# Optimization experiments

Hardware: AMD Instinct MI355X
Metric: run time of the kernel (lower is better)

Reference implementation:

```python
import jax, jax.numpy as jnp
import numpy as np

W, H = 1920, 1080
WEIGHT = 0.2          # self.weight
CONT_W = 0.1          # continuity_weight
RANK_M = 1e-4         # ranking_margin
CONT_M = 1e-4         # continuity_margin
SAMPLE_RATIO = 0.25
R = 3                 # knn_crop_radius
PAD_VAL = -1000000.0


def setup_inputs() -> dict:
    key = jax.random.key(0)
    k1, k2, k3 = jax.random.split(key, 3)
    return {
        "target_depths": jax.random.uniform(k1, (1, H * W), dtype=jnp.float32) * 100.0,
        "render_depths": jax.random.uniform(k2, (H * W,), dtype=jnp.float32) * 100.0,
        "valid_mask": jax.random.randint(k3, (1, H * W, 1), 0, 2, dtype=jnp.int32),
        "width": W,
        "height": H,
    }


def _sample_depth_loss_indices(depths, width, height, valid_mask, n_samples,
                               rank_patch_size, r, key):
    win = 2 * r + 1                      # 7
    top_n = int(0.3 * win * win + 1)     # 15
    ks = jax.random.split(key, 5)
    sy = jax.random.randint(ks[0], (n_samples, 1), 0, height - rank_patch_size)
    sx = jax.random.randint(ks[1], (n_samples, 1), 0, width - rank_patch_size)
    sy = sy + jax.random.randint(ks[2], (n_samples, 2), 0, rank_patch_size)
    sx = sx + jax.random.randint(ks[3], (n_samples, 2), 0, rank_patch_size)
    sample_idx = sy * width + sx                               # (n, 2)
    sampled_depth = depths[0][sample_idx]                      # (n, 2)

    padded = jnp.pad(depths.reshape(height, width), r, constant_values=PAD_VAL)
    dy = jnp.repeat(jnp.arange(win), win)                      # (49,) row offsets
    dx = jnp.tile(jnp.arange(win), win)                        # (49,) col offsets
    # padded coords: (y - r + dy) + r == y + dy
    py = sy[..., None] + dy                                    # (n, 2, 49)
    px = sx[..., None] + dx
    depth_crops = padded[py, px]                               # (n, 2, 49)

    sorted_crop_idx = jnp.argsort(jnp.abs(depth_crops - sampled_depth[..., None]), axis=-1)
    nbr_sample = jax.random.randint(ks[4], (n_samples, 2, 1), 1, top_n)
    rel = jnp.take_along_axis(sorted_crop_idx, nbr_sample, axis=-1)[..., 0]  # (n, 2)
    ny = sy - r + rel // win
    nx = sx - r + rel % win
    neighbours_idx = ny * width + nx                           # (n, 2)

    vm = valid_mask[0].astype(bool)                            # (H*W, C)
    samples_mask = vm[sample_idx].any(-1).all(-1)              # (n,)
    neighbours_mask = vm[neighbours_idx].any(-1).all(-1)
    full_mask = samples_mask & neighbours_mask

    # per-pair descending sort by sampled target depth
    order = jnp.argsort(-sampled_depth, axis=-1)
    s_sorted = jnp.take_along_axis(sample_idx, order, axis=-1)
    n_sorted = jnp.take_along_axis(neighbours_idx, order, axis=-1)
    idx4 = jnp.concatenate([s_sorted, n_sorted], axis=-1)      # (n, 4)
    return idx4, full_mask


def reference(target_depths, render_depths, valid_mask, width, height):
    n_samples = int(width * height * SAMPLE_RATIO)
    rank_patch_size = width // 8
    idx4, mask = _sample_depth_loss_indices(
        target_depths, width, height, valid_mask, n_samples, rank_patch_size,
        R, jax.random.key(42))
    d = render_depths[idx4].reshape(-1, 2, 2)                  # (n, 2, 2)
    rank = jnp.maximum(d[:, 0, 0] - d[:, 0, 1] + RANK_M, 0.0)  # (n,)
    cont = jnp.maximum(jnp.abs(d[:, 0, :] - d[:, 1, :]) - CONT_M, 0.0)  # (n, 2)
    # masked means == torch's boolean filtering followed by .mean()
    m = mask.astype(rank.dtype)
    denom = jnp.maximum(m.sum(), 1.0)
    rank_mean = (rank * m).sum() / denom
    cont_mean = (cont * m[:, None]).sum() / (denom * 2.0)
    return jnp.stack([WEIGHT * rank_mean, WEIGHT * CONT_W * cont_mean])
```

## Files before the change

### kernel.cpp

```cpp
#include <hip/hip_runtime.h>
#include <stdint.h>


#define IMG_W 1920
#define IMG_H 1080
#define N_SAMP 518400
#define PAD_VAL (-1000000.0f)

struct Keys { uint32_t k[5][2][2]; };

static __host__ __device__ inline void tf2x32(uint32_t k0, uint32_t k1,
                                              uint32_t x0, uint32_t x1,
                                              uint32_t& o0, uint32_t& o1)
{
  const uint32_t ks2 = k0 ^ k1 ^ 0x1BD11BDAu;
  x0 += k0; x1 += k1;
#define TFR(r) { x0 += x1; x1 = (x1 << (r)) | (x1 >> (32 - (r))); x1 ^= x0; }
  TFR(13) TFR(15) TFR(26) TFR(6)
  x0 += k1;  x1 += ks2 + 1u;
  TFR(17) TFR(29) TFR(16) TFR(24)
  x0 += ks2; x1 += k0 + 2u;
  TFR(13) TFR(15) TFR(26) TFR(6)
  x0 += k0;  x1 += k1 + 3u;
  TFR(17) TFR(29) TFR(16) TFR(24)
  x0 += k1;  x1 += ks2 + 4u;
  TFR(13) TFR(15) TFR(26) TFR(6)
  x0 += ks2; x1 += k0 + 5u;
#undef TFR
  o0 = x0; o1 = x1;
}

__device__ __forceinline__ uint32_t jrbits(const uint32_t kk[2], uint32_t f)
{
  uint32_t a, b;
  tf2x32(kk[0], kk[1], 0u, f, a, b);
  return a ^ b;
}

__device__ __forceinline__ uint32_t jrandint(const Keys& K, int r, uint32_t f,
                                             uint32_t span)
{
  const uint32_t hi = jrbits(K.k[r][0], f);
  const uint32_t lo = jrbits(K.k[r][1], f);
  uint32_t m = 65536u % span;
  m = (m * m) % span;
  return ((hi % span) * m + (lo % span)) % span;
}

static void compute_keys(Keys& K)
{
  uint32_t ks[5][2];
  for (uint32_t t = 0; t < 5; t++) {
    uint32_t a, b; tf2x32(0u, 42u, 0u, t, a, b);
    ks[t][0] = a; ks[t][1] = b;
  }
  for (int r = 0; r < 5; r++) {
    uint32_t a, b;
    tf2x32(ks[r][0], ks[r][1], 0u, 0u, a, b); K.k[r][0][0] = a; K.k[r][0][1] = b;
    tf2x32(ks[r][0], ks[r][1], 0u, 1u, a, b); K.k[r][1][0] = a; K.k[r][1][1] = b;
  }
}

__device__ __forceinline__ int crop_neighbor(const float* __restrict__ tgt,
                                             int sy, int sx, float sd,
                                             uint32_t nbr)
{
  float v[7][8];
  const bool interior = (sy >= 3) && (sy <= IMG_H - 4) &&
                        (sx >= 3) && (sx <= IMG_W - 4);
  if (interior) {
    const float* p = tgt + (sy - 3) * IMG_W + (sx - 3);
#pragma unroll
    for (int r = 0; r < 7; r++)
#pragma unroll
      for (int c = 0; c < 8; c++)
        v[r][c] = p[r * IMG_W + c];
  } else {
#pragma unroll
    for (int r = 0; r < 7; r++) {
      const int yy = sy - 3 + r;
      const bool rok = (yy >= 0) && (yy < IMG_H);
#pragma unroll
      for (int c = 0; c < 8; c++) {
        const int xx = sx - 3 + c;
        const bool ok = rok && (c < 7) && (xx >= 0) && (xx < IMG_W);
        v[r][c] = ok ? tgt[yy * IMG_W + xx] : PAD_VAL;
      }
    }
  }

  uint32_t arr[15];
#pragma unroll
  for (int t = 0; t < 15; t++) arr[t] = 0xFFFFFFFFu;

#pragma unroll
  for (int r = 0; r < 7; r++) {
#pragma unroll
    for (int c = 0; c < 7; c++) {
      const int q = r * 7 + c;
      uint32_t key = (__float_as_uint(v[r][c] - sd) & 0x7FFFFFC0u) | (uint32_t)q;
      const int depth = (q + 1 < 15) ? (q + 1) : 15;
#pragma unroll
      for (int t = 0; t < 15; t++) {
        if (t < depth) {
          const uint32_t lo = min(key, arr[t]);
          const uint32_t hi = max(key, arr[t]);
          arr[t] = lo; key = hi;
        }
      }
    }
  }

  uint32_t relkey = 0;
#pragma unroll
  for (int t = 1; t < 15; t++)
    if ((uint32_t)t == nbr) relkey = arr[t];
  const uint32_t rel = relkey & 63u;
  const int ny = sy - 3 + (int)(rel / 7u);
  const int nx = sx - 3 + (int)(rel % 7u);
  return ny * IMG_W + nx;
}

__global__ __launch_bounds__(256, 2) void gs_fused(
    const float* __restrict__ tgt,
    const float* __restrict__ rnd,
    const int*   __restrict__ vmask,
    float* __restrict__ acc,
    Keys K)
{
  __shared__ unsigned long long ent[256];
  __shared__ float    res_sd[512];
  __shared__ int      res_ni[512];
  __shared__ uint32_t scnt[4];
  __shared__ float    partial[12];

  const uint32_t tid  = threadIdx.x;
  const uint32_t lane = tid & 63u;
  const uint32_t wave = tid >> 6;
  const uint32_t ui   = blockIdx.x * 256u + tid;

  const uint32_t syb = jrandint(K, 0, ui, 840u);
  const uint32_t sxb = jrandint(K, 1, ui, 1680u);
  const uint32_t sy0 = syb + jrandint(K, 2, 2u * ui,      240u);
  const uint32_t sy1 = syb + jrandint(K, 2, 2u * ui + 1u, 240u);
  const uint32_t sx0 = sxb + jrandint(K, 3, 2u * ui,      240u);
  const uint32_t sx1 = sxb + jrandint(K, 3, 2u * ui + 1u, 240u);
  const bool ok = (vmask[sy0 * IMG_W + sx0] != 0) &&
                  (vmask[sy1 * IMG_W + sx1] != 0);

  const unsigned long long ball = __ballot(ok);
  if (lane == 0) scnt[wave] = (uint32_t)__popcll(ball);
  __syncthreads();

  uint32_t base = 0;
#pragma unroll
  for (uint32_t w = 0; w < 4; w++) if (w < wave) base += scnt[w];
  const uint32_t nsurv = scnt[0] + scnt[1] + scnt[2] + scnt[3];

  if (ok) {
    const uint32_t pos = base + (uint32_t)__popcll(ball & ((1ull << lane) - 1ull));
    ent[pos] = ((unsigned long long)ui  << 44) |
               ((unsigned long long)sy0 << 33) | ((unsigned long long)sx0 << 22) |
               ((unsigned long long)sy1 << 11) |  (unsigned long long)sx1;
  }
  __syncthreads();

  for (uint32_t t = tid; t < 2u * nsurv; t += 256u) {
    const unsigned long long e = ent[t >> 1];
    const int jj = (int)(t & 1u);
    const uint32_t eui = (uint32_t)(e >> 44);
    const int sy = jj ? (int)((e >> 11) & 2047u) : (int)((e >> 33) & 2047u);
    const int sx = jj ? (int)( e        & 2047u) : (int)((e >> 22) & 2047u);

    const float sd = tgt[sy * IMG_W + sx];
    const uint32_t nbr = 1u + jrandint(K, 4, 2u * eui + (uint32_t)jj, 14u);
    const int nidx = crop_neighbor(tgt, sy, sx, sd, nbr);
    res_sd[t] = sd;
    res_ni[t] = (vmask[nidx] != 0) ? nidx : -1;
  }
  __syncthreads();

  float rank_c = 0.f, cont_c = 0.f, cnt_c = 0.f;
  for (uint32_t s = tid; s < nsurv; s += 256u) {
    const int n0 = res_ni[2u * s], n1 = res_ni[2u * s + 1u];
    if ((n0 >= 0) && (n1 >= 0)) {
      const unsigned long long e = ent[s];
      const int esy0 = (int)((e >> 33) & 2047u), esx0 = (int)((e >> 22) & 2047u);
      const int esy1 = (int)((e >> 11) & 2047u), esx1 = (int)( e        & 2047u);
      const float r0 = rnd[esy0 * IMG_W + esx0];
      const float r1 = rnd[esy1 * IMG_W + esx1];
      const float q0 = rnd[n0], q1 = rnd[n1];
      const float sd0 = res_sd[2u * s], sd1 = res_sd[2u * s + 1u];
      const bool keep = sd0 >= sd1;
      const float ra = keep ? r0 : r1;
      const float rb = keep ? r1 : r0;
      rank_c += fmaxf(ra - rb + 1e-4f, 0.f);
      cont_c += fmaxf(fabsf(r0 - q0) - 1e-4f, 0.f)
              + fmaxf(fabsf(r1 - q1) - 1e-4f, 0.f);
      cnt_c  += 1.f;
    }
  }

#pragma unroll
  for (int off = 32; off > 0; off >>= 1) {
    rank_c += __shfl_down(rank_c, off);
    cont_c += __shfl_down(cont_c, off);
    cnt_c  += __shfl_down(cnt_c, off);
  }
  if (lane == 0) {
    partial[wave * 3 + 0] = rank_c;
    partial[wave * 3 + 1] = cont_c;
    partial[wave * 3 + 2] = cnt_c;
  }
  __syncthreads();
  if (tid < 3) {
    const float s = partial[tid] + partial[3 + tid] +
                    partial[6 + tid] + partial[9 + tid];
    atomicAdd(acc + tid, s);
  }
}

__global__ void gs_finalize(const float* __restrict__ acc, float* __restrict__ out)
{
  const float denom = fmaxf(acc[2], 1.0f);
  out[0] = 0.2f * (acc[0] / denom);
  out[1] = 0.2f * 0.1f * (acc[1] / (denom * 2.0f));
}

extern "C" void kernel_launch(void* const* d_in, const int* in_sizes, int n_in,
                              void* d_out, int out_size, void* d_ws, size_t ws_size,
                              hipStream_t stream)
{
  (void)in_sizes; (void)n_in; (void)out_size; (void)ws_size;
  const float* tgt   = (const float*)d_in[0];
  const float* rnd   = (const float*)d_in[1];
  const int*   vmask = (const int*)d_in[2];
  float* out = (float*)d_out;
  float* acc = (float*)d_ws;

  Keys K;
  compute_keys(K);

  hipMemsetAsync(acc, 0, 16, stream);
  gs_fused<<<N_SAMP / 256, 256, 0, stream>>>(tgt, rnd, vmask, acc, K);
  gs_finalize<<<1, 1, 0, stream>>>(acc, out);
}
```

Baseline: 62.69 us.

## Bitpack valid mask and process two sample batches per block

```diff
diff --git a/kernel.cpp b/kernel.cpp
--- a/kernel.cpp
+++ b/kernel.cpp
@@ -4,6 +4,7 @@
 
 #define IMG_W 1920
 #define IMG_H 1080
+#define N_PIX (IMG_W * IMG_H)
 #define N_SAMP 518400
 #define PAD_VAL (-1000000.0f)
 
@@ -61,20 +62,34 @@
   }
 }
 
+__device__ __forceinline__ bool validat(const unsigned long long* __restrict__ vb,
+                                        const int* __restrict__ vm, uint32_t idx)
+{
+  if (vb) return ((vb[idx >> 6] >> (idx & 63u)) & 1ull) != 0ull;
+  return vm[idx] != 0;
+}
+
+__global__ __launch_bounds__(256) void gs_bitpack(
+    const int* __restrict__ vmask,
+    unsigned long long* __restrict__ vbits)
+{
+  const uint32_t gid = blockIdx.x * 256u + threadIdx.x;
+  const unsigned long long ball = __ballot(vmask[gid] != 0);
+  if ((threadIdx.x & 63u) == 0) vbits[gid >> 6] = ball;
+}
+
 __device__ __forceinline__ int crop_neighbor(const float* __restrict__ tgt,
                                              int sy, int sx, float sd,
                                              uint32_t nbr)
 {
   float v[7][8];
   const bool interior = (sy >= 3) && (sy <= IMG_H - 4) &&
-                        (sx >= 3) && (sx <= IMG_W - 4);
+                        (sx >= 3) && (sx <= IMG_W - 5);
   if (interior) {
     const float* p = tgt + (sy - 3) * IMG_W + (sx - 3);
 #pragma unroll
     for (int r = 0; r < 7; r++)
-#pragma unroll
-      for (int c = 0; c < 8; c++)
-        v[r][c] = p[r * IMG_W + c];
+      __builtin_memcpy(&v[r][0], p + r * IMG_W, 32);
   } else {
 #pragma unroll
     for (int r = 0; r < 7; r++) {
@@ -83,11 +98,12 @@
 #pragma unroll
       for (int c = 0; c < 8; c++) {
         const int xx = sx - 3 + c;
-        const bool ok = rok && (c < 7) && (xx >= 0) && (xx < IMG_W);
-        v[r][c] = ok ? tgt[yy * IMG_W + xx] : PAD_VAL;
+        const bool okc = rok && (c < 7) && (xx >= 0) && (xx < IMG_W);
+        v[r][c] = okc ? tgt[yy * IMG_W + xx] : PAD_VAL;
       }
     }
   }
+  __builtin_amdgcn_sched_barrier(0);
 
   uint32_t arr[15];
 #pragma unroll
@@ -125,58 +141,76 @@
     const float* __restrict__ tgt,
     const float* __restrict__ rnd,
     const int*   __restrict__ vmask,
+    const unsigned long long* __restrict__ vbits,
     float* __restrict__ acc,
     Keys K)
 {
-  __shared__ unsigned long long ent[256];
-  __shared__ float    res_sd[512];
-  __shared__ int      res_ni[512];
-  __shared__ uint32_t scnt[4];
+  __shared__ unsigned long long ent[512];
+  __shared__ float    res_sd[1024];
+  __shared__ int      res_ni[1024];
+  __shared__ uint32_t scnt[8];
   __shared__ float    partial[12];
 
   const uint32_t tid  = threadIdx.x;
   const uint32_t lane = tid & 63u;
   const uint32_t wave = tid >> 6;
-  const uint32_t ui   = blockIdx.x * 256u + tid;
-
-  const uint32_t syb = jrandint(K, 0, ui, 840u);
-  const uint32_t sxb = jrandint(K, 1, ui, 1680u);
-  const uint32_t sy0 = syb + jrandint(K, 2, 2u * ui,      240u);
-  const uint32_t sy1 = syb + jrandint(K, 2, 2u * ui + 1u, 240u);
-  const uint32_t sx0 = sxb + jrandint(K, 3, 2u * ui,      240u);
-  const uint32_t sx1 = sxb + jrandint(K, 3, 2u * ui + 1u, 240u);
-  const bool ok = (vmask[sy0 * IMG_W + sx0] != 0) &&
-                  (vmask[sy1 * IMG_W + sx1] != 0);
-
-  const unsigned long long ball = __ballot(ok);
-  if (lane == 0) scnt[wave] = (uint32_t)__popcll(ball);
-  __syncthreads();
-
-  uint32_t base = 0;
-#pragma unroll
-  for (uint32_t w = 0; w < 4; w++) if (w < wave) base += scnt[w];
-  const uint32_t nsurv = scnt[0] + scnt[1] + scnt[2] + scnt[3];
-
-  if (ok) {
-    const uint32_t pos = base + (uint32_t)__popcll(ball & ((1ull << lane) - 1ull));
-    ent[pos] = ((unsigned long long)ui  << 44) |
-               ((unsigned long long)sy0 << 33) | ((unsigned long long)sx0 << 22) |
-               ((unsigned long long)sy1 << 11) |  (unsigned long long)sx1;
-  }
+
+  unsigned long long e[2];
+  bool ok[2];
+#pragma unroll
+  for (int h = 0; h < 2; h++) {
+    const uint32_t ui = blockIdx.x * 512u + (uint32_t)h * 256u + tid;
+    bool o = false;
+    unsigned long long ee = 0;
+    if (ui < N_SAMP) {
+      const uint32_t syb = jrandint(K, 0, ui, 840u);
+      const uint32_t sxb = jrandint(K, 1, ui, 1680u);
+      const uint32_t sy0 = syb + jrandint(K, 2, 2u * ui,      240u);
+      const uint32_t sy1 = syb + jrandint(K, 2, 2u * ui + 1u, 240u);
+      const uint32_t sx0 = sxb + jrandint(K, 3, 2u * ui,      240u);
+      const uint32_t sx1 = sxb + jrandint(K, 3, 2u * ui + 1u, 240u);
+      o = validat(vbits, vmask, sy0 * IMG_W + sx0) &&
+          validat(vbits, vmask, sy1 * IMG_W + sx1);
+      ee = ((unsigned long long)ui  << 44) |
+           ((unsigned long long)sy0 << 33) | ((unsigned long long)sx0 << 22) |
+           ((unsigned long long)sy1 << 11) |  (unsigned long long)sx1;
+    }
+    ok[h] = o; e[h] = ee;
+  }
+
+  const unsigned long long b0 = __ballot(ok[0]);
+  const unsigned long long b1 = __ballot(ok[1]);
+  if (lane == 0) {
+    scnt[wave]     = (uint32_t)__popcll(b0);
+    scnt[4 + wave] = (uint32_t)__popcll(b1);
+  }
+  __syncthreads();
+
+  uint32_t base0 = 0, sum0 = 0, base1 = 0, nsurv = 0;
+#pragma unroll
+  for (uint32_t w = 0; w < 4; w++) {
+    if (w < wave) { base0 += scnt[w]; base1 += scnt[4 + w]; }
+    sum0  += scnt[w];
+    nsurv += scnt[w] + scnt[4 + w];
+  }
+  base1 += sum0;
+
+  if (ok[0]) ent[base0 + (uint32_t)__popcll(b0 & ((1ull << lane) - 1ull))] = e[0];
+  if (ok[1]) ent[base1 + (uint32_t)__popcll(b1 & ((1ull << lane) - 1ull))] = e[1];
   __syncthreads();
 
   for (uint32_t t = tid; t < 2u * nsurv; t += 256u) {
-    const unsigned long long e = ent[t >> 1];
+    const unsigned long long ee = ent[t >> 1];
     const int jj = (int)(t & 1u);
-    const uint32_t eui = (uint32_t)(e >> 44);
-    const int sy = jj ? (int)((e >> 11) & 2047u) : (int)((e >> 33) & 2047u);
-    const int sx = jj ? (int)( e        & 2047u) : (int)((e >> 22) & 2047u);
+    const uint32_t eui = (uint32_t)(ee >> 44);
+    const int sy = jj ? (int)((ee >> 11) & 2047u) : (int)((ee >> 33) & 2047u);
+    const int sx = jj ? (int)( ee        & 2047u) : (int)((ee >> 22) & 2047u);
 
     const float sd = tgt[sy * IMG_W + sx];
     const uint32_t nbr = 1u + jrandint(K, 4, 2u * eui + (uint32_t)jj, 14u);
     const int nidx = crop_neighbor(tgt, sy, sx, sd, nbr);
     res_sd[t] = sd;
-    res_ni[t] = (vmask[nidx] != 0) ? nidx : -1;
+    res_ni[t] = validat(vbits, vmask, (uint32_t)nidx) ? nidx : -1;
   }
   __syncthreads();
 
@@ -184,9 +218,9 @@
   for (uint32_t s = tid; s < nsurv; s += 256u) {
     const int n0 = res_ni[2u * s], n1 = res_ni[2u * s + 1u];
     if ((n0 >= 0) && (n1 >= 0)) {
-      const unsigned long long e = ent[s];
-      const int esy0 = (int)((e >> 33) & 2047u), esx0 = (int)((e >> 22) & 2047u);
-      const int esy1 = (int)((e >> 11) & 2047u), esx1 = (int)( e        & 2047u);
+      const unsigned long long ee = ent[s];
+      const int esy0 = (int)((ee >> 33) & 2047u), esx0 = (int)((ee >> 22) & 2047u);
+      const int esy1 = (int)((ee >> 11) & 2047u), esx1 = (int)( ee        & 2047u);
       const float r0 = rnd[esy0 * IMG_W + esx0];
       const float r1 = rnd[esy1 * IMG_W + esx1];
       const float q0 = rnd[n0], q1 = rnd[n1];
@@ -231,17 +265,27 @@
                               void* d_out, int out_size, void* d_ws, size_t ws_size,
                               hipStream_t stream)
 {
-  (void)in_sizes; (void)n_in; (void)out_size; (void)ws_size;
+  (void)in_sizes; (void)n_in; (void)out_size;
   const float* tgt   = (const float*)d_in[0];
   const float* rnd   = (const float*)d_in[1];
   const int*   vmask = (const int*)d_in[2];
   float* out = (float*)d_out;
+
   float* acc = (float*)d_ws;
+  unsigned long long* vbits = (unsigned long long*)((char*)d_ws + 16);
+  const size_t need = 16 + (size_t)(N_PIX / 64) * 8;
 
   Keys K;
   compute_keys(K);
 
   hipMemsetAsync(acc, 0, 16, stream);
-  gs_fused<<<N_SAMP / 256, 256, 0, stream>>>(tgt, rnd, vmask, acc, K);
+
+  const bool use_bits = (ws_size >= need);
+  if (use_bits)
+    gs_bitpack<<<N_PIX / 256, 256, 0, stream>>>(vmask, vbits);
+
+  const int blocksF = (N_SAMP + 511) / 512;
+  gs_fused<<<blocksF, 256, 0, stream>>>(tgt, rnd, vmask,
+                                        use_bits ? vbits : nullptr, acc, K);
   gs_finalize<<<1, 1, 0, stream>>>(acc, out);
 }
```

Result: faster. 60.42 us (-3.6%).

## Split into bitpack, sample-compaction and crop kernels with packed valid mask

Applied to the files above, without the earlier changes.

```diff
diff --git a/kernel.cpp b/kernel.cpp
--- a/kernel.cpp
+++ b/kernel.cpp
@@ -4,8 +4,11 @@
 
 #define IMG_W 1920
 #define IMG_H 1080
+#define N_PIX (IMG_W * IMG_H)
 #define N_SAMP 518400
 #define PAD_VAL (-1000000.0f)
+
+typedef float f32x4 __attribute__((ext_vector_type(4)));
 
 struct Keys { uint32_t k[5][2][2]; };
 
@@ -61,20 +64,35 @@
   }
 }
 
+__device__ __forceinline__ bool bittest(const unsigned long long* __restrict__ vb,
+                                        uint32_t idx)
+{
+  return ((vb[idx >> 6] >> (idx & 63u)) & 1ull) != 0ull;
+}
+
+__global__ __launch_bounds__(256) void gs_bitpack(
+    const int* __restrict__ vmask,
+    unsigned long long* __restrict__ vbits)
+{
+  const uint32_t gid = blockIdx.x * 256u + threadIdx.x;
+  const unsigned long long ball = __ballot(vmask[gid] != 0);
+  if ((threadIdx.x & 63u) == 0) vbits[gid >> 6] = ball;
+}
+
 __device__ __forceinline__ int crop_neighbor(const float* __restrict__ tgt,
                                              int sy, int sx, float sd,
                                              uint32_t nbr)
 {
-  float v[7][8];
+  f32x4 A[7], B[7];
   const bool interior = (sy >= 3) && (sy <= IMG_H - 4) &&
-                        (sx >= 3) && (sx <= IMG_W - 4);
+                        (sx >= 3) && (sx <= IMG_W - 5);
   if (interior) {
     const float* p = tgt + (sy - 3) * IMG_W + (sx - 3);
 #pragma unroll
-    for (int r = 0; r < 7; r++)
-#pragma unroll
-      for (int c = 0; c < 8; c++)
-        v[r][c] = p[r * IMG_W + c];
+    for (int r = 0; r < 7; r++) {
+      __builtin_memcpy(&A[r], p + r * IMG_W,     16);
+      __builtin_memcpy(&B[r], p + r * IMG_W + 4, 16);
+    }
   } else {
 #pragma unroll
     for (int r = 0; r < 7; r++) {
@@ -83,11 +101,16 @@
 #pragma unroll
       for (int c = 0; c < 8; c++) {
         const int xx = sx - 3 + c;
-        const bool ok = rok && (c < 7) && (xx >= 0) && (xx < IMG_W);
-        v[r][c] = ok ? tgt[yy * IMG_W + xx] : PAD_VAL;
+        const bool okc = rok && (c < 7) && (xx >= 0) && (xx < IMG_W);
+        const float v = okc ? tgt[yy * IMG_W + xx] : PAD_VAL;
+        if (c < 4) A[r][c] = v; else B[r][c - 4] = v;
       }
     }
   }
+  asm volatile("" ::
+      "v"(A[0]), "v"(A[1]), "v"(A[2]), "v"(A[3]), "v"(A[4]), "v"(A[5]), "v"(A[6]),
+      "v"(B[0]), "v"(B[1]), "v"(B[2]), "v"(B[3]), "v"(B[4]), "v"(B[5]), "v"(B[6]));
+  __builtin_amdgcn_sched_barrier(0);
 
   uint32_t arr[15];
 #pragma unroll
@@ -95,10 +118,12 @@
 
 #pragma unroll
   for (int r = 0; r < 7; r++) {
+    const float vals[8] = { A[r][0], A[r][1], A[r][2], A[r][3],
+                            B[r][0], B[r][1], B[r][2], B[r][3] };
 #pragma unroll
     for (int c = 0; c < 7; c++) {
       const int q = r * 7 + c;
-      uint32_t key = (__float_as_uint(v[r][c] - sd) & 0x7FFFFFC0u) | (uint32_t)q;
+      uint32_t key = (__float_as_uint(vals[c] - sd) & 0x7FFFFFC0u) | (uint32_t)q;
       const int depth = (q + 1 < 15) ? (q + 1) : 15;
 #pragma unroll
       for (int t = 0; t < 15; t++) {
@@ -116,9 +141,124 @@
   for (int t = 1; t < 15; t++)
     if ((uint32_t)t == nbr) relkey = arr[t];
   const uint32_t rel = relkey & 63u;
-  const int ny = sy - 3 + (int)(rel / 7u);
-  const int nx = sx - 3 + (int)(rel % 7u);
-  return ny * IMG_W + nx;
+  return (sy - 3 + (int)(rel / 7u)) * IMG_W + (sx - 3 + (int)(rel % 7u));
+}
+
+__global__ __launch_bounds__(256) void gs_sample(
+    const unsigned long long* __restrict__ vbits,
+    uint32_t* __restrict__ wcount,
+    unsigned long long* __restrict__ wlist,
+    Keys K)
+{
+  __shared__ unsigned long long ent[256];
+  __shared__ uint32_t scnt[4];
+  __shared__ uint32_t gbase_s;
+
+  const uint32_t tid  = threadIdx.x;
+  const uint32_t lane = tid & 63u;
+  const uint32_t wave = tid >> 6;
+  const uint32_t ui   = blockIdx.x * 256u + tid;
+
+  const uint32_t syb = jrandint(K, 0, ui, 840u);
+  const uint32_t sxb = jrandint(K, 1, ui, 1680u);
+  const uint32_t sy0 = syb + jrandint(K, 2, 2u * ui,      240u);
+  const uint32_t sy1 = syb + jrandint(K, 2, 2u * ui + 1u, 240u);
+  const uint32_t sx0 = sxb + jrandint(K, 3, 2u * ui,      240u);
+  const uint32_t sx1 = sxb + jrandint(K, 3, 2u * ui + 1u, 240u);
+  const bool ok = bittest(vbits, sy0 * IMG_W + sx0) &&
+                  bittest(vbits, sy1 * IMG_W + sx1);
+
+  const unsigned long long ball = __ballot(ok);
+  if (lane == 0) scnt[wave] = (uint32_t)__popcll(ball);
+  __syncthreads();
+
+  uint32_t base = 0;
+#pragma unroll
+  for (uint32_t w = 0; w < 4; w++) if (w < wave) base += scnt[w];
+  const uint32_t nsurv = scnt[0] + scnt[1] + scnt[2] + scnt[3];
+
+  if (ok) {
+    const uint32_t nbr0 = 1u + jrandint(K, 4, 2u * ui,      14u);
+    const uint32_t nbr1 = 1u + jrandint(K, 4, 2u * ui + 1u, 14u);
+    const uint32_t pos = base + (uint32_t)__popcll(ball & ((1ull << lane) - 1ull));
+    ent[pos] = ((unsigned long long)nbr1 << 48) | ((unsigned long long)nbr0 << 44) |
+               ((unsigned long long)sy0  << 33) | ((unsigned long long)sx0  << 22) |
+               ((unsigned long long)sy1  << 11) |  (unsigned long long)sx1;
+  }
+  if (tid == 0 && nsurv) gbase_s = atomicAdd(wcount, nsurv);
+  __syncthreads();
+
+  const uint32_t gbase = gbase_s;
+  for (uint32_t t = tid; t < nsurv; t += 256u)
+    wlist[gbase + t] = ent[t];
+}
+
+__global__ __launch_bounds__(256, 4) void gs_crop(
+    const float* __restrict__ tgt,
+    const float* __restrict__ rnd,
+    const unsigned long long* __restrict__ vbits,
+    const uint32_t* __restrict__ wcount,
+    const unsigned long long* __restrict__ wlist,
+    float* __restrict__ acc)
+{
+  const uint32_t n2 = 2u * *wcount;
+  if (blockIdx.x * 256u >= n2) return;
+
+  __shared__ float partial[12];
+  const uint32_t tid  = threadIdx.x;
+  const uint32_t lane = tid & 63u;
+  const uint32_t wave = tid >> 6;
+  const uint32_t t = blockIdx.x * 256u + tid;
+
+  float sd = 0.f, r = 0.f, q = 0.f;
+  bool v = false;
+  if (t < n2) {
+    const unsigned long long e = wlist[t >> 1];
+    const int j = (int)(t & 1u);
+    const int sy  = j ? (int)((e >> 11) & 2047u) : (int)((e >> 33) & 2047u);
+    const int sx  = j ? (int)( e        & 2047u) : (int)((e >> 22) & 2047u);
+    const uint32_t nbr = j ? (uint32_t)((e >> 48) & 15u)
+                           : (uint32_t)((e >> 44) & 15u);
+    const int sidx = sy * IMG_W + sx;
+    sd = tgt[sidx];
+    r  = rnd[sidx];
+    const int nidx = crop_neighbor(tgt, sy, sx, sd, nbr);
+    v = bittest(vbits, (uint32_t)nidx);
+    q = rnd[nidx];
+  }
+
+  const float psd = __shfl_xor(sd, 1);
+  const float pr  = __shfl_xor(r, 1);
+  const bool  pv  = (bool)__shfl_xor((int)v, 1);
+  const bool pairok = (t < n2) && v && pv;
+
+  float cont_c = pairok ? fmaxf(fabsf(r - q) - 1e-4f, 0.f) : 0.f;
+  float rank_c = 0.f, cnt_c = 0.f;
+  if (pairok && ((t & 1u) == 0)) {
+    const bool keep = sd >= psd;
+    const float ra = keep ? r : pr;
+    const float rb = keep ? pr : r;
+    rank_c = fmaxf(ra - rb + 1e-4f, 0.f);
+    cnt_c = 1.f;
+  }
+
+#pragma unroll
+  for (int off = 32; off > 0; off >>= 1) {
+    rank_c += __shfl_down(rank_c, off);
+    cont_c += __shfl_down(cont_c, off);
+    cnt_c  += __shfl_down(cnt_c, off);
+  }
+  if (lane == 0) {
+    partial[wave * 3 + 0] = rank_c;
+    partial[wave * 3 + 1] = cont_c;
+    partial[wave * 3 + 2] = cnt_c;
+  }
+  __syncthreads();
+  if (tid < 3) {
+    const float s = partial[tid] + partial[3 + tid] +
+                    partial[6 + tid] + partial[9 + tid];
+    atomicAdd(acc + tid, s);
+  }
 }
 
 __global__ __launch_bounds__(256, 2) void gs_fused(
@@ -128,79 +268,48 @@
     float* __restrict__ acc,
     Keys K)
 {
-  __shared__ unsigned long long ent[256];
-  __shared__ float    res_sd[512];
-  __shared__ int      res_ni[512];
-  __shared__ uint32_t scnt[4];
-  __shared__ float    partial[12];
-
+  __shared__ float partial[12];
   const uint32_t tid  = threadIdx.x;
   const uint32_t lane = tid & 63u;
   const uint32_t wave = tid >> 6;
   const uint32_t ui   = blockIdx.x * 256u + tid;
 
-  const uint32_t syb = jrandint(K, 0, ui, 840u);
-  const uint32_t sxb = jrandint(K, 1, ui, 1680u);
-  const uint32_t sy0 = syb + jrandint(K, 2, 2u * ui,      240u);
-  const uint32_t sy1 = syb + jrandint(K, 2, 2u * ui + 1u, 240u);
-  const uint32_t sx0 = sxb + jrandint(K, 3, 2u * ui,      240u);
-  const uint32_t sx1 = sxb + jrandint(K, 3, 2u * ui + 1u, 240u);
-  const bool ok = (vmask[sy0 * IMG_W + sx0] != 0) &&
-                  (vmask[sy1 * IMG_W + sx1] != 0);
-
-  const unsigned long long ball = __ballot(ok);
-  if (lane == 0) scnt[wave] = (uint32_t)__popcll(ball);
-  __syncthreads();
-
-  uint32_t base = 0;
-#pragma unroll
-  for (uint32_t w = 0; w < 4; w++) if (w < wave) base += scnt[w];
-  const uint32_t nsurv = scnt[0] + scnt[1] + scnt[2] + scnt[3];
-
-  if (ok) {
-    const uint32_t pos = base + (uint32_t)__popcll(ball & ((1ull << lane) - 1ull));
-    ent[pos] = ((unsigned long long)ui  << 44) |
-               ((unsigned long long)sy0 << 33) | ((unsigned long long)sx0 << 22) |
-               ((unsigned long long)sy1 << 11) |  (unsigned long long)sx1;
-  }
-  __syncthreads();
-
-  for (uint32_t t = tid; t < 2u * nsurv; t += 256u) {
-    const unsigned long long e = ent[t >> 1];
-    const int jj = (int)(t & 1u);
-    const uint32_t eui = (uint32_t)(e >> 44);
-    const int sy = jj ? (int)((e >> 11) & 2047u) : (int)((e >> 33) & 2047u);
-    const int sx = jj ? (int)( e        & 2047u) : (int)((e >> 22) & 2047u);
-
-    const float sd = tgt[sy * IMG_W + sx];
-    const uint32_t nbr = 1u + jrandint(K, 4, 2u * eui + (uint32_t)jj, 14u);
-    const int nidx = crop_neighbor(tgt, sy, sx, sd, nbr);
-    res_sd[t] = sd;
-    res_ni[t] = (vmask[nidx] != 0) ? nidx : -1;
-  }
-  __syncthreads();
-
   float rank_c = 0.f, cont_c = 0.f, cnt_c = 0.f;
-  for (uint32_t s = tid; s < nsurv; s += 256u) {
-    const int n0 = res_ni[2u * s], n1 = res_ni[2u * s + 1u];
-    if ((n0 >= 0) && (n1 >= 0)) {
-      const unsigned long long e = ent[s];
-      const int esy0 = (int)((e >> 33) & 2047u), esx0 = (int)((e >> 22) & 2047u);
-      const int esy1 = (int)((e >> 11) & 2047u), esx1 = (int)( e        & 2047u);
-      const float r0 = rnd[esy0 * IMG_W + esx0];
-      const float r1 = rnd[esy1 * IMG_W + esx1];
-      const float q0 = rnd[n0], q1 = rnd[n1];
-      const float sd0 = res_sd[2u * s], sd1 = res_sd[2u * s + 1u];
-      const bool keep = sd0 >= sd1;
-      const float ra = keep ? r0 : r1;
-      const float rb = keep ? r1 : r0;
-      rank_c += fmaxf(ra - rb + 1e-4f, 0.f);
-      cont_c += fmaxf(fabsf(r0 - q0) - 1e-4f, 0.f)
-              + fmaxf(fabsf(r1 - q1) - 1e-4f, 0.f);
-      cnt_c  += 1.f;
-    }
-  }
-
+  if (ui < N_SAMP) {
+    const uint32_t syb = jrandint(K, 0, ui, 840u);
+    const uint32_t sxb = jrandint(K, 1, ui, 1680u);
+    int sy[2], sx[2], sidx[2];
+    float sd[2];
+    bool sm = true;
+#pragma unroll
+    for (int j = 0; j < 2; j++) {
+      sy[j] = (int)(syb + jrandint(K, 2, 2u * ui + (uint32_t)j, 240u));
+      sx[j] = (int)(sxb + jrandint(K, 3, 2u * ui + (uint32_t)j, 240u));
+      sidx[j] = sy[j] * IMG_W + sx[j];
+      sd[j] = tgt[sidx[j]];
+      sm = sm && (vmask[sidx[j]] != 0);
+    }
+    if (sm) {
+      int nidx[2]; bool nm = true;
+#pragma unroll
+      for (int j = 0; j < 2; j++) {
+        const uint32_t nbr = 1u + jrandint(K, 4, 2u * ui + (uint32_t)j, 14u);
+        nidx[j] = crop_neighbor(tgt, sy[j], sx[j], sd[j], nbr);
+        nm = nm && (vmask[nidx[j]] != 0);
+      }
+      if (nm) {
+        const float r0 = rnd[sidx[0]], r1 = rnd[sidx[1]];
+        const float q0 = rnd[nidx[0]], q1 = rnd[nidx[1]];
+        const bool keep = sd[0] >= sd[1];
+        const float ra = keep ? r0 : r1;
+        const float rb = keep ? r1 : r0;
+        rank_c = fmaxf(ra - rb + 1e-4f, 0.f);
+        cont_c = fmaxf(fabsf(r0 - q0) - 1e-4f, 0.f)
+               + fmaxf(fabsf(r1 - q1) - 1e-4f, 0.f);
+        cnt_c = 1.f;
+      }
+    }
+  }
 #pragma unroll
   for (int off = 32; off > 0; off >>= 1) {
     rank_c += __shfl_down(rank_c, off);
@@ -231,17 +340,31 @@
                               void* d_out, int out_size, void* d_ws, size_t ws_size,
                               hipStream_t stream)
 {
-  (void)in_sizes; (void)n_in; (void)out_size; (void)ws_size;
+  (void)in_sizes; (void)n_in; (void)out_size;
   const float* tgt   = (const float*)d_in[0];
   const float* rnd   = (const float*)d_in[1];
   const int*   vmask = (const int*)d_in[2];
   float* out = (float*)d_out;
-  float* acc = (float*)d_ws;
+
+  float*    acc    = (float*)d_ws;
+  uint32_t* wcount = (uint32_t*)d_ws + 3;
+  unsigned long long* vbits = (unsigned long long*)((char*)d_ws + 16);
+  unsigned long long* wlist =
+      (unsigned long long*)((char*)d_ws + 16 + (size_t)(N_PIX / 64) * 8);
+  const size_t need = 16 + (size_t)(N_PIX / 64) * 8 + (size_t)N_SAMP * 8;
 
   Keys K;
   compute_keys(K);
 
-  hipMemsetAsync(acc, 0, 16, stream);
-  gs_fused<<<N_SAMP / 256, 256, 0, stream>>>(tgt, rnd, vmask, acc, K);
+  hipMemsetAsync(d_ws, 0, 16, stream);
+
+  if (ws_size >= need) {
+    gs_bitpack<<<N_PIX / 256, 256, 0, stream>>>(vmask, vbits);
+    gs_sample<<<N_SAMP / 256, 256, 0, stream>>>(vbits, wcount, wlist, K);
+    gs_crop<<<(2 * N_SAMP + 255) / 256, 256, 0, stream>>>(
+        tgt, rnd, vbits, wcount, wlist, acc);
+  } else {
+    gs_fused<<<N_SAMP / 256, 256, 0, stream>>>(tgt, rnd, vmask, acc, K);
+  }
   gs_finalize<<<1, 1, 0, stream>>>(acc, out);
 }
```

Measured after the change: 79.90 us. 27.5% more time.
